# Performance work log

Measured on AMD Instinct MI355X. Metric: run time of the kernel, lower is better.

Reference implementation:

```python
import jax, jax.numpy as jnp
import numpy as np

E = 64            # embedding_size
N = 131072        # total nodes (64 states x 2048 objects)
B = 64            # number of states (for readout)
NUM_LAYERS = 2
SMOOTH = 12.0     # MAXIMUM_SMOOTHNESS
RELS = (("r1", 1, 400_000), ("r2", 2, 400_000), ("r3", 3, 150_000))  # (name, arity, n_atoms)


def mish(x):
    return x * jnp.tanh(jax.nn.softplus(x))


def mlp(x, Wi, bi, Wo, bo):
    # MLP: outer(mish(inner(x)))
    return mish(x @ Wi + bi) @ Wo + bo


def setup_inputs() -> dict:
    key = jax.random.key(0)
    ks = iter(jax.random.split(key, 64))

    def lin(i, o):
        s = 1.0 / np.sqrt(i)
        return jax.random.uniform(next(ks), (i, o), jnp.float32, -s, s)

    d = {"node_embeddings": jax.random.normal(next(ks), (N, E), jnp.float32)}
    for r, a, m in RELS:
        d[f"atoms_{r}"] = jax.random.randint(next(ks), (m * a,), 0, N, jnp.int32)
    d["token_sizes"] = jnp.full((B,), N // B, jnp.int32)
    for r, a, _ in RELS:
        sz = a * E
        d[f"Wi_{r}"] = lin(sz, sz); d[f"bi_{r}"] = jnp.zeros((sz,), jnp.float32)
        d[f"Wo_{r}"] = lin(sz, sz); d[f"bo_{r}"] = jnp.zeros((sz,), jnp.float32)
    d["uWi"] = lin(2 * E, 2 * E); d["ubi"] = jnp.zeros((2 * E,), jnp.float32)
    d["uWo"] = lin(2 * E, E);     d["ubo"] = jnp.zeros((E,), jnp.float32)
    for p in ("v", "d"):
        d[f"{p}Wi"] = lin(E, E); d[f"{p}bi"] = jnp.zeros((E,), jnp.float32)
        d[f"{p}Wo"] = lin(E, 1); d[f"{p}bo"] = jnp.zeros((1,), jnp.float32)
    return d


def _layer(h, atoms, rp, uWi, ubi, uWo, ubo):
    # per-relation gather -> residual MLP -> flatten back to per-term messages
    msg_list, idx_list = [], []
    for (r, a, _) in RELS:
        idx = atoms[r]                                  # [m*a] int node ids
        Wi, bi, Wo, bo = rp[r]
        x = h[idx].reshape(-1, a * E)                   # [m, a*E]
        y = x + mlp(x, Wi, bi, Wo, bo)                  # residual relation MLP
        msg_list.append(y.reshape(-1, E))               # [m*a, E]
        idx_list.append(idx)
    msgs = jnp.concatenate(msg_list, 0)                 # [T, E]
    idxs = jnp.concatenate(idx_list, 0)                 # [T]

    # smooth-max aggregation (torch: index_reduce amax under no_grad + stabilized exp-sum-log)
    cnt = jax.ops.segment_sum(jnp.ones((idxs.shape[0], 1), msgs.dtype), idxs, num_segments=N)
    seg_max = jax.ops.segment_max(msgs, idxs, num_segments=N)     # -inf for empty segments
    exps_max = jax.lax.stop_gradient(jnp.where(cnt > 0, seg_max, 0.0))  # include_self=False; empty nodes stay 0
    exps = jnp.exp(SMOOTH * (msgs - exps_max[idxs]))
    exps_sum = 1e-16 + jax.ops.segment_sum(exps, idxs, num_segments=N)
    max_msg = jnp.log(exps_sum) / SMOOTH + exps_max     # [N, E]

    return h + mlp(jnp.concatenate([max_msg, h], 1), uWi, ubi, uWo, ubo)


def _readout(h, token_sizes, Wi, bi, Wo, bo):
    # SumReadout: cumsum-diff segment sums over states, then MLP -> scalar per state
    ci = jnp.cumsum(token_sizes) - 1
    cs = jnp.cumsum(h, axis=0)[ci]                      # [B, E] cumulative sums at segment ends
    agg = jnp.concatenate([cs[:1], cs[1:] - cs[:-1]], 0)
    return mlp(agg, Wi, bi, Wo, bo).reshape(-1)


def _forward(node_embeddings, atoms, token_sizes, params):
    (rp, uWi, ubi, uWo, ubo, vWi, vbi, vWo, vbo, dWi, dbi, dWo, dbo) = params
    h = node_embeddings
    for _ in range(NUM_LAYERS):
        h = _layer(h, atoms, rp, uWi, ubi, uWo, ubo)
    values = _readout(h, token_sizes, vWi, vbi, vWo, vbo)
    deadends = _readout(h, token_sizes, dWi, dbi, dWo, dbo)
    return values, deadends


def reference(node_embeddings, atoms_r1, atoms_r2, atoms_r3, token_sizes,
              Wi_r1, bi_r1, Wo_r1, bo_r1,
              Wi_r2, bi_r2, Wo_r2, bo_r2,
              Wi_r3, bi_r3, Wo_r3, bo_r3,
              uWi, ubi, uWo, ubo,
              vWi, vbi, vWo, vbo,
              dWi, dbi, dWo, dbo):
    atoms = {"r1": atoms_r1, "r2": atoms_r2, "r3": atoms_r3}
    rp = {"r1": (Wi_r1, bi_r1, Wo_r1, bo_r1),
          "r2": (Wi_r2, bi_r2, Wo_r2, bo_r2),
          "r3": (Wi_r3, bi_r3, Wo_r3, bo_r3)}
    params = (rp, uWi, ubi, uWo, ubo, vWi, vbi, vWo, vbo, dWi, dbi, dWo, dbo)
    return _forward(node_embeddings, atoms, token_sizes, params)
```

## Files before the change

### kernel.cpp

```cpp
#include <hip/hip_runtime.h>
#include <math.h>

#define N_NODES 131072
#define NSTATES 64
#define NH ((size_t)N_NODES * 64)

typedef short bf16x8 __attribute__((ext_vector_type(8)));
typedef float f32x4 __attribute__((ext_vector_type(4)));

__device__ __forceinline__ ushort f2bf(float f) {
    unsigned u = __float_as_uint(f);
    return (ushort)((u + 0x7fffu + ((u >> 16) & 1u)) >> 16);
}
__device__ __forceinline__ float bf2f(ushort h) {
    return __uint_as_float(((unsigned)h) << 16);
}
__device__ __forceinline__ float mishf(float x) {
    if (x > 30.f) return x;
    float t = __builtin_amdgcn_exp2f(1.4426950408889634f * x);
    float r = t * t + 2.f * t;
    return x * r * __builtin_amdgcn_rcpf(r + 2.f);
}
__device__ __forceinline__ unsigned enc_f(float f) {
    unsigned u = __float_as_uint(f);
    return (u & 0x80000000u) ? ~u : (u | 0x80000000u);
}
__device__ __forceinline__ float dec_f(unsigned k) {
    unsigned u = (k & 0x80000000u) ? (k & 0x7fffffffu) : ~k;
    return __uint_as_float(u);
}

__device__ __forceinline__ bf16x8 load8f(const float* p) {
    const float4* q = (const float4*)p;
    float4 v0 = q[0], v1 = q[1];
    bf16x8 u;
    u[0] = (short)f2bf(v0.x); u[1] = (short)f2bf(v0.y);
    u[2] = (short)f2bf(v0.z); u[3] = (short)f2bf(v0.w);
    u[4] = (short)f2bf(v1.x); u[5] = (short)f2bf(v1.y);
    u[6] = (short)f2bf(v1.z); u[7] = (short)f2bf(v1.w);
    return u;
}

__global__ __launch_bounds__(256) void h2bf_kernel(
    const float* __restrict__ h, ushort* __restrict__ hb)
{
    size_t i = ((size_t)blockIdx.x * 256 + threadIdx.x) * 8;
    if (i >= NH) return;
    *(bf16x8*)(hb + i) = load8f(h + i);
}

struct WtJob  { const float* src; ushort* dst; int K; int Nc; int start; };
struct WtJobs { WtJob j[8]; int total; };

__global__ __launch_bounds__(256) void wt_conv_all_kernel(WtJobs jobs)
{
    int i = blockIdx.x * 256 + threadIdx.x;
    if (i >= jobs.total) return;
    int jj = 0;
    #pragma unroll
    for (int k = 1; k < 8; k++) if (i >= jobs.j[k].start) jj = k;
    WtJob jb = jobs.j[jj];
    int local = i - jb.start;
    int o = local / jb.K, k = local % jb.K;
    jb.dst[(size_t)o * jb.K + k] = f2bf(jb.src[(size_t)k * jb.Nc + o]);
}

__global__ __launch_bounds__(256) void count_kernel(
    const int* __restrict__ atoms, int T, unsigned* __restrict__ cnt)
{
    int i = blockIdx.x * 256 + threadIdx.x;
    if (i < T) atomicAdd(&cnt[atoms[i]], 1u);
}

__global__ __launch_bounds__(256) void scan1_kernel(
    const unsigned* __restrict__ cnt, unsigned* __restrict__ base,
    unsigned* __restrict__ totals)
{
    __shared__ unsigned sm[256];
    int t = threadIdx.x, blk = blockIdx.x;
    int i0 = blk * 512;
    unsigned a = cnt[i0 + 2 * t], bb = cnt[i0 + 2 * t + 1];
    unsigned p = a + bb;
    sm[t] = p;
    __syncthreads();
    for (int off = 1; off < 256; off <<= 1) {
        unsigned v = (t >= off) ? sm[t - off] : 0u;
        __syncthreads();
        sm[t] += v;
        __syncthreads();
    }
    unsigned incl = sm[t];
    base[i0 + 2 * t]     = incl - p;
    base[i0 + 2 * t + 1] = incl - p + a;
    if (t == 255) totals[blk] = sm[255];
}

__global__ __launch_bounds__(256) void scan2_kernel(
    unsigned* __restrict__ base, unsigned* __restrict__ pos,
    const unsigned* __restrict__ totals)
{
    __shared__ unsigned ps[4];
    int t = threadIdx.x, blk = blockIdx.x;
    int lane = t & 63, wv = t >> 6;
    unsigned v = (t < blk) ? totals[t] : 0u;
    #pragma unroll
    for (int o = 32; o >= 1; o >>= 1) v += (unsigned)__shfl_xor((int)v, o);
    if (lane == 0) ps[wv] = v;
    __syncthreads();
    unsigned off = ps[0] + ps[1] + ps[2] + ps[3];
    int i0 = blk * 512;
    unsigned b0 = base[i0 + 2 * t] + off;
    unsigned b1 = base[i0 + 2 * t + 1] + off;
    base[i0 + 2 * t]     = b0;  pos[i0 + 2 * t]     = b0;
    base[i0 + 2 * t + 1] = b1;  pos[i0 + 2 * t + 1] = b1;
}

template<int ARITY, int MODE>
__global__ __launch_bounds__(256, (ARITY == 3) ? 3 : 4)
void rel_kernel(const ushort* __restrict__ h, const int* __restrict__ atoms,
                const ushort* __restrict__ WiT, const float* __restrict__ bi,
                const ushort* __restrict__ WoT, const float* __restrict__ bo,
                unsigned* __restrict__ pos, ushort* __restrict__ y_sorted,
                unsigned* __restrict__ enc, float* __restrict__ exps, int m)
{
    constexpr int AE  = ARITY * 64;
    constexpr int BM  = 64;
    constexpr int NTW = AE / 64;
    constexpr int KS  = AE / 32;
    constexpr int S   = AE * 2;
    __shared__ __align__(16) ushort xs[BM * AE];
    __shared__ __align__(16) ushort ts[BM * AE];
    __shared__ unsigned slot_sm[BM * ARITY];
    const int tid = threadIdx.x, lane = tid & 63, wv = tid >> 6;
    const int a0 = blockIdx.x * BM;

    for (int task = tid; task < BM * (AE / 8); task += 256) {
        int r  = task / (AE / 8);
        int c8 = task % (AE / 8);
        int atom = a0 + r;
        bf16x8 u = {0, 0, 0, 0, 0, 0, 0, 0};
        if (atom < m) {
            int node = atoms[atom * ARITY + (c8 >> 3)];
            u = *(const bf16x8*)(h + (size_t)node * 64 + (size_t)(c8 & 7) * 8);
        }
        *(bf16x8*)((char*)xs + r * S + ((c8 * 16) ^ ((r & 7) << 4))) = u;
    }
    __syncthreads();

    const int cw0 = wv * NTW * 16;
    const int kg  = (lane >> 4) * 8;
    const int cl  = lane & 15;

    f32x4 acc[4][NTW];
    #pragma unroll
    for (int n = 0; n < NTW; n++) {
        float b = bi[cw0 + n * 16 + cl];
        #pragma unroll
        for (int a = 0; a < 4; a++) acc[a][n] = (f32x4){b, b, b, b};
    }
    #pragma unroll
    for (int ks = 0; ks < KS; ks++) {
        bf16x8 bf[NTW];
        #pragma unroll
        for (int n = 0; n < NTW; n++)
            bf[n] = *(const bf16x8*)(WiT + (size_t)(cw0 + n * 16 + cl) * AE + ks * 32 + kg);
        #pragma unroll
        for (int a = 0; a < 4; a++) {
            int row = a * 16 + cl;
            bf16x8 af = *(const bf16x8*)((char*)xs + row * S + (((ks * 32 + kg) * 2) ^ ((row & 7) << 4)));
            #pragma unroll
            for (int n = 0; n < NTW; n++)
                acc[a][n] = __builtin_amdgcn_mfma_f32_16x16x32_bf16(af, bf[n], acc[a][n], 0, 0, 0);
        }
    }
    #pragma unroll
    for (int a = 0; a < 4; a++)
        #pragma unroll
        for (int n = 0; n < NTW; n++)
            #pragma unroll
            for (int j = 0; j < 4; j++) {
                int row = a * 16 + (lane >> 4) * 4 + j;
                int col = cw0 + n * 16 + cl;
                *(ushort*)((char*)ts + row * S + ((col * 2) ^ ((row & 7) << 4))) = f2bf(mishf(acc[a][n][j]));
            }
    __syncthreads();

    #pragma unroll
    for (int n = 0; n < NTW; n++) {
        float b = bo[cw0 + n * 16 + cl];
        #pragma unroll
        for (int a = 0; a < 4; a++) acc[a][n] = (f32x4){b, b, b, b};
    }
    #pragma unroll
    for (int ks = 0; ks < KS; ks++) {
        bf16x8 bf[NTW];
        #pragma unroll
        for (int n = 0; n < NTW; n++)
            bf[n] = *(const bf16x8*)(WoT + (size_t)(cw0 + n * 16 + cl) * AE + ks * 32 + kg);
        #pragma unroll
        for (int a = 0; a < 4; a++) {
            int row = a * 16 + cl;
            bf16x8 af = *(const bf16x8*)((char*)ts + row * S + (((ks * 32 + kg) * 2) ^ ((row & 7) << 4)));
            #pragma unroll
            for (int n = 0; n < NTW; n++)
                acc[a][n] = __builtin_amdgcn_mfma_f32_16x16x32_bf16(af, bf[n], acc[a][n], 0, 0, 0);
        }
    }
    #pragma unroll
    for (int a = 0; a < 4; a++)
        #pragma unroll
        for (int n = 0; n < NTW; n++)
            #pragma unroll
            for (int j = 0; j < 4; j++) {
                int row = a * 16 + (lane >> 4) * 4 + j;
                int col = cw0 + n * 16 + cl;
                ushort* xp = (ushort*)((char*)xs + row * S + ((col * 2) ^ ((row & 7) << 4)));
                *xp = f2bf(bf2f(*xp) + acc[a][n][j]);
            }
    __syncthreads();

    const int nrows = BM * ARITY;
    if (MODE == 0) {
        if (tid < nrows) {
            int grow = a0 * ARITY + tid;
            unsigned s = 0u;
            if (grow < m * ARITY) s = atomicAdd(&pos[atoms[grow]], 1u);
            slot_sm[tid] = s;
        }
        __syncthreads();
        for (int rr = wv; rr < nrows; rr += 4) {
            int grow = a0 * ARITY + rr;
            if (grow >= m * ARITY) break;
            int r = rr / ARITY, c = (rr % ARITY) * 64 + lane;
            ushort yu = *(ushort*)((char*)xs + r * S + ((c * 2) ^ ((r & 7) << 4)));
            y_sorted[(size_t)slot_sm[rr] * 64 + lane] = yu;
        }
    } else {
        for (int rr = wv; rr < nrows; rr += 4) {
            int grow = a0 * ARITY + rr;
            if (grow >= m * ARITY) break;
            int node = atoms[grow];
            int r = rr / ARITY, c = (rr % ARITY) * 64 + lane;
            ushort yu = *(ushort*)((char*)xs + r * S + ((c * 2) ^ ((r & 7) << 4)));
            if (MODE == 1) {
                atomicMax(&enc[(size_t)node * 64 + lane], enc_f(bf2f(yu)));
            } else {
                size_t cell = (size_t)node * 64 + lane;
                float mx = dec_f(enc[cell]);
                atomicAdd(&exps[cell], __builtin_amdgcn_exp2f(17.312340490667562f * (bf2f(yu) - mx)));
            }
        }
    }
}

__global__ __launch_bounds__(256) void aggregate_kernel(
    const ushort* __restrict__ y_sorted, const unsigned* __restrict__ base,
    const unsigned* __restrict__ cnt, unsigned* __restrict__ pos,
    ushort* __restrict__ mm)
{
    int node = blockIdx.x * 4 + (threadIdx.x >> 6);
    int lane = threadIdx.x & 63;
    unsigned b = base[node], c = cnt[node];
    if (lane == 0) pos[node] = b;
    const ushort* p = y_sorted + (size_t)b * 64 + lane;
    float mx = -3.402823466e38f;
    for (unsigned j = 0; j < c; j++)
        mx = fmaxf(mx, bf2f(p[(size_t)j * 64]));
    float me = c ? mx : 0.f;
    float s = 0.f;
    for (unsigned j = 0; j < c; j++)
        s += __builtin_amdgcn_exp2f(17.312340490667562f * (bf2f(p[(size_t)j * 64]) - me));
    float r = __builtin_amdgcn_logf(1e-16f + s) * 0.05776226504666211f + me;
    mm[(size_t)node * 64 + lane] = f2bf(r);
}

__global__ __launch_bounds__(256) void finalize_mm_kernel(
    const unsigned* __restrict__ enc, const float* __restrict__ exps,
    ushort* __restrict__ mm)
{
    size_t i = (size_t)blockIdx.x * 256 + threadIdx.x;
    if (i >= NH) return;
    unsigned key = enc[i];
    float mx = key ? dec_f(key) : 0.f;
    float r = __builtin_amdgcn_logf(1e-16f + exps[i]) * 0.05776226504666211f + mx;
    mm[i] = f2bf(r);
}

__global__ __launch_bounds__(256, 4)
void update_kernel(ushort* __restrict__ hio, const ushort* __restrict__ mm,
                   const ushort* __restrict__ uWiT, const float* __restrict__ ubi,
                   const ushort* __restrict__ uWoT, const float* __restrict__ ubo)
{
    constexpr int AE = 128, BM = 64, S = 256, NTW = 2, KS = 4;
    __shared__ __align__(16) ushort xs[BM * AE];
    __shared__ __align__(16) ushort ts[BM * AE];
    const int tid = threadIdx.x, lane = tid & 63, wv = tid >> 6;
    const int n0 = blockIdx.x * BM;

    for (int task = tid; task < BM * 16; task += 256) {
        int r = task >> 4, c8 = task & 15;
        int node = n0 + r;
        bf16x8 u;
        if (c8 < 8) u = *(const bf16x8*)(mm  + (size_t)node * 64 + c8 * 8);
        else        u = *(const bf16x8*)(hio + (size_t)node * 64 + (size_t)(c8 - 8) * 8);
        *(bf16x8*)((char*)xs + r * S + ((c8 * 16) ^ ((r & 7) << 4))) = u;
    }
    __syncthreads();

    const int cw0 = wv * NTW * 16;
    const int kg  = (lane >> 4) * 8;
    const int cl  = lane & 15;

    f32x4 acc[4][NTW];
    #pragma unroll
    for (int n = 0; n < NTW; n++) {
        float b = ubi[cw0 + n * 16 + cl];
        #pragma unroll
        for (int a = 0; a < 4; a++) acc[a][n] = (f32x4){b, b, b, b};
    }
    #pragma unroll
    for (int ks = 0; ks < KS; ks++) {
        bf16x8 bf[NTW];
        #pragma unroll
        for (int n = 0; n < NTW; n++)
            bf[n] = *(const bf16x8*)(uWiT + (size_t)(cw0 + n * 16 + cl) * AE + ks * 32 + kg);
        #pragma unroll
        for (int a = 0; a < 4; a++) {
            int row = a * 16 + cl;
            bf16x8 af = *(const bf16x8*)((char*)xs + row * S + (((ks * 32 + kg) * 2) ^ ((row & 7) << 4)));
            #pragma unroll
            for (int n = 0; n < NTW; n++)
                acc[a][n] = __builtin_amdgcn_mfma_f32_16x16x32_bf16(af, bf[n], acc[a][n], 0, 0, 0);
        }
    }
    #pragma unroll
    for (int a = 0; a < 4; a++)
        #pragma unroll
        for (int n = 0; n < NTW; n++)
            #pragma unroll
            for (int j = 0; j < 4; j++) {
                int row = a * 16 + (lane >> 4) * 4 + j;
                int col = cw0 + n * 16 + cl;
                *(ushort*)((char*)ts + row * S + ((col * 2) ^ ((row & 7) << 4))) = f2bf(mishf(acc[a][n][j]));
            }
    __syncthreads();

    f32x4 acc2[4];
    {
        float b = ubo[wv * 16 + cl];
        #pragma unroll
        for (int a = 0; a < 4; a++) acc2[a] = (f32x4){b, b, b, b};
    }
    #pragma unroll
    for (int ks = 0; ks < KS; ks++) {
        bf16x8 bf = *(const bf16x8*)(uWoT + (size_t)(wv * 16 + cl) * AE + ks * 32 + kg);
        #pragma unroll
        for (int a = 0; a < 4; a++) {
            int row = a * 16 + cl;
            bf16x8 af = *(const bf16x8*)((char*)ts + row * S + (((ks * 32 + kg) * 2) ^ ((row & 7) << 4)));
            acc2[a] = __builtin_amdgcn_mfma_f32_16x16x32_bf16(af, bf, acc2[a], 0, 0, 0);
        }
    }
    #pragma unroll
    for (int a = 0; a < 4; a++)
        #pragma unroll
        for (int j = 0; j < 4; j++) {
            int row = a * 16 + (lane >> 4) * 4 + j;
            int col = wv * 16 + cl;
            int hc = 64 + col;
            float hold = bf2f(*(ushort*)((char*)xs + row * S + ((hc * 2) ^ ((row & 7) << 4))));
            hio[(size_t)(n0 + row) * 64 + col] = f2bf(hold + acc2[a][j]);
        }
}

__global__ __launch_bounds__(64) void offsets_kernel(
    const int* __restrict__ toksz, int* __restrict__ off)
{
    int lane = threadIdx.x;
    int v = toksz[lane];
    int inc = v;
    #pragma unroll
    for (int o = 1; o < 64; o <<= 1) {
        int t = __shfl_up(inc, o);
        if (lane >= o) inc += t;
    }
    off[lane] = inc - v;
}

#define RCHUNK 32
__global__ __launch_bounds__(256) void readout_partial_kernel(
    const ushort* __restrict__ h, const int* __restrict__ toksz,
    const int* __restrict__ off, float* __restrict__ part)
{
    int s = blockIdx.x >> 5, c = blockIdx.x & (RCHUNK - 1);
    int cntr = toksz[s];
    int rpc = (cntr + RCHUNK - 1) / RCHUNK;
    int r0 = c * rpc;
    int r1 = min(r0 + rpc, cntr);
    int col = threadIdx.x & 63, rg = threadIdx.x >> 6;
    int base = off[s];
    float acc = 0.f;
    for (int r = r0 + rg; r < r1; r += 4)
        acc += bf2f(h[(size_t)(base + r) * 64 + col]);
    __shared__ float red[4][64];
    red[rg][col] = acc;
    __syncthreads();
    if (rg == 0)
        part[(size_t)blockIdx.x * 64 + col] = red[0][col] + red[1][col] + red[2][col] + red[3][col];
}

__global__ __launch_bounds__(256) void readout_reduce_kernel(
    const float* __restrict__ part, float* __restrict__ agg)
{
    int s = blockIdx.x;
    int col = threadIdx.x & 63, rg = threadIdx.x >> 6;
    float acc = 0.f;
    for (int k = rg; k < RCHUNK; k += 4)
        acc += part[(size_t)(s * RCHUNK + k) * 64 + col];
    __shared__ float red[4][64];
    red[rg][col] = acc;
    __syncthreads();
    if (rg == 0)
        agg[s * 64 + col] = red[0][col] + red[1][col] + red[2][col] + red[3][col];
}

__global__ __launch_bounds__(64) void readout_mlp_kernel(
    const float* __restrict__ agg,
    const float* __restrict__ vWi, const float* __restrict__ vbi,
    const float* __restrict__ vWo, const float* __restrict__ vbo,
    const float* __restrict__ dWi, const float* __restrict__ dbi,
    const float* __restrict__ dWo, const float* __restrict__ dbo,
    float* __restrict__ out)
{
    int s = blockIdx.x;
    int lane = threadIdx.x;
    float accv = vbi[lane], accd = dbi[lane];
    for (int k = 0; k < 64; k++) {
        float a = agg[s * 64 + k];
        accv = fmaf(a, vWi[k * 64 + lane], accv);
        accd = fmaf(a, dWi[k * 64 + lane], accd);
    }
    float pv = mishf(accv) * vWo[lane];
    float pd = mishf(accd) * dWo[lane];
    #pragma unroll
    for (int o = 1; o < 64; o <<= 1) {
        pv += __shfl_xor(pv, o);
        pd += __shfl_xor(pd, o);
    }
    if (lane == 0) { out[s] = pv + vbo[0]; out[64 + s] = pd + dbo[0]; }
}

extern "C" void kernel_launch(void* const* d_in, const int* in_sizes, int n_in,
                              void* d_out, int out_size, void* d_ws, size_t ws_size,
                              hipStream_t stream)
{
    const float* h0   = (const float*)d_in[0];
    const int* atoms1 = (const int*)d_in[1];
    const int* atoms2 = (const int*)d_in[2];
    const int* atoms3 = (const int*)d_in[3];
    const int* tsizes = (const int*)d_in[4];
    const float* Wi1 = (const float*)d_in[5],  *bi1 = (const float*)d_in[6];
    const float* Wo1 = (const float*)d_in[7],  *bo1 = (const float*)d_in[8];
    const float* Wi2 = (const float*)d_in[9],  *bi2 = (const float*)d_in[10];
    const float* Wo2 = (const float*)d_in[11], *bo2 = (const float*)d_in[12];
    const float* Wi3 = (const float*)d_in[13], *bi3 = (const float*)d_in[14];
    const float* Wo3 = (const float*)d_in[15], *bo3 = (const float*)d_in[16];
    const float* uWi = (const float*)d_in[17], *ubi = (const float*)d_in[18];
    const float* uWo = (const float*)d_in[19], *ubo = (const float*)d_in[20];
    const float* vWi = (const float*)d_in[21], *vbi = (const float*)d_in[22];
    const float* vWo = (const float*)d_in[23], *vbo = (const float*)d_in[24];
    const float* dWi = (const float*)d_in[25], *dbi = (const float*)d_in[26];
    const float* dWo = (const float*)d_in[27], *dbo = (const float*)d_in[28];
    float* out = (float*)d_out;

    const int rows1 = in_sizes[1];
    const int rows2 = in_sizes[2];
    const int rows3 = in_sizes[3];
    const int m1 = rows1, m2 = rows2 / 2, m3 = rows3 / 3;
    const int T = rows1 + rows2 + rows3;

    char* w = (char*)d_ws;
    auto alloc = [&](size_t bytes) { char* p = w; w += (bytes + 255) & ~(size_t)255; return p; };
    ushort* h1       = (ushort*)alloc(NH * 2);
    ushort* mm       = (ushort*)alloc(NH * 2);
    unsigned* cnt    = (unsigned*)alloc(N_NODES * 4);
    unsigned* base   = (unsigned*)alloc(N_NODES * 4);
    unsigned* pos    = (unsigned*)alloc(N_NODES * 4);
    unsigned* totals = (unsigned*)alloc(256 * 4);
    float* agg       = (float*)alloc(NSTATES * 64 * 4);
    float* part      = (float*)alloc((size_t)NSTATES * RCHUNK * 64 * 4);
    int* roff        = (int*)alloc(NSTATES * 4);
    ushort* WiT1 = (ushort*)alloc(64 * 64 * 2);
    ushort* WoT1 = (ushort*)alloc(64 * 64 * 2);
    ushort* WiT2 = (ushort*)alloc(128 * 128 * 2);
    ushort* WoT2 = (ushort*)alloc(128 * 128 * 2);
    ushort* WiT3 = (ushort*)alloc(192 * 192 * 2);
    ushort* WoT3 = (ushort*)alloc(192 * 192 * 2);
    ushort* uWiT = (ushort*)alloc(128 * 128 * 2);
    ushort* uWoT = (ushort*)alloc(64 * 128 * 2);
    char* tail = w;

    size_t y_bytes  = (size_t)T * 64 * 2;
    const bool csr  = ((size_t)(tail - (char*)d_ws) + ((y_bytes + 255) & ~(size_t)255)) <= ws_size;
    ushort* y_sorted = nullptr;
    unsigned* enc = nullptr;
    float* exps = nullptr;
    if (csr) {
        y_sorted = (ushort*)alloc(y_bytes);
    } else {
        enc  = (unsigned*)alloc(NH * 4);
        exps = (float*)alloc(NH * 4);
    }

    h2bf_kernel<<<(int)(NH / 8 / 256), 256, 0, stream>>>(h0, h1);

    {
        WtJobs jobs;
        int s = 0;
        auto add = [&](int idx, const float* src, ushort* dst, int K, int Nc) {
            jobs.j[idx] = {src, dst, K, Nc, s};
            s += K * Nc;
        };
        add(0, Wi1, WiT1, 64, 64);
        add(1, Wo1, WoT1, 64, 64);
        add(2, Wi2, WiT2, 128, 128);
        add(3, Wo2, WoT2, 128, 128);
        add(4, Wi3, WiT3, 192, 192);
        add(5, Wo3, WoT3, 192, 192);
        add(6, uWi, uWiT, 128, 128);
        add(7, uWo, uWoT, 128, 64);
        jobs.total = s;
        wt_conv_all_kernel<<<(s + 255) / 256, 256, 0, stream>>>(jobs);
    }

    if (csr) {
        hipMemsetAsync(cnt, 0, N_NODES * 4, stream);
        count_kernel<<<(rows1 + 255) / 256, 256, 0, stream>>>(atoms1, rows1, cnt);
        count_kernel<<<(rows2 + 255) / 256, 256, 0, stream>>>(atoms2, rows2, cnt);
        count_kernel<<<(rows3 + 255) / 256, 256, 0, stream>>>(atoms3, rows3, cnt);
        scan1_kernel<<<256, 256, 0, stream>>>(cnt, base, totals);
        scan2_kernel<<<256, 256, 0, stream>>>(base, pos, totals);
    }

    const int g1 = (m1 + 63) / 64, g2 = (m2 + 63) / 64, g3 = (m3 + 63) / 64;

    for (int layer = 0; layer < 2; layer++) {
        if (csr) {
            rel_kernel<1, 0><<<g1, 256, 0, stream>>>(h1, atoms1, WiT1, bi1, WoT1, bo1, pos, y_sorted, nullptr, nullptr, m1);
            rel_kernel<2, 0><<<g2, 256, 0, stream>>>(h1, atoms2, WiT2, bi2, WoT2, bo2, pos, y_sorted, nullptr, nullptr, m2);
            rel_kernel<3, 0><<<g3, 256, 0, stream>>>(h1, atoms3, WiT3, bi3, WoT3, bo3, pos, y_sorted, nullptr, nullptr, m3);
            aggregate_kernel<<<N_NODES / 4, 256, 0, stream>>>(y_sorted, base, cnt, pos, mm);
        } else {
            hipMemsetAsync(enc, 0, NH * 8, stream);
            rel_kernel<1, 1><<<g1, 256, 0, stream>>>(h1, atoms1, WiT1, bi1, WoT1, bo1, nullptr, nullptr, enc, exps, m1);
            rel_kernel<2, 1><<<g2, 256, 0, stream>>>(h1, atoms2, WiT2, bi2, WoT2, bo2, nullptr, nullptr, enc, exps, m2);
            rel_kernel<3, 1><<<g3, 256, 0, stream>>>(h1, atoms3, WiT3, bi3, WoT3, bo3, nullptr, nullptr, enc, exps, m3);
            rel_kernel<1, 2><<<g1, 256, 0, stream>>>(h1, atoms1, WiT1, bi1, WoT1, bo1, nullptr, nullptr, enc, exps, m1);
            rel_kernel<2, 2><<<g2, 256, 0, stream>>>(h1, atoms2, WiT2, bi2, WoT2, bo2, nullptr, nullptr, enc, exps, m2);
            rel_kernel<3, 2><<<g3, 256, 0, stream>>>(h1, atoms3, WiT3, bi3, WoT3, bo3, nullptr, nullptr, enc, exps, m3);
            finalize_mm_kernel<<<(int)((NH + 255) / 256), 256, 0, stream>>>(enc, exps, mm);
        }
        update_kernel<<<N_NODES / 64, 256, 0, stream>>>(h1, mm, uWiT, ubi, uWoT, ubo);
    }

    offsets_kernel<<<1, 64, 0, stream>>>(tsizes, roff);
    readout_partial_kernel<<<NSTATES * RCHUNK, 256, 0, stream>>>(h1, tsizes, roff, part);
    readout_reduce_kernel<<<NSTATES, 256, 0, stream>>>(part, agg);
    readout_mlp_kernel<<<NSTATES, 64, 0, stream>>>(agg, vWi, vbi, vWo, vbo,
                                                   dWi, dbi, dWo, dbo, out);
}
```

Measured before the change: 829.5 us.

## Precompute CSR slots once and use online-softmax vectorized aggregation

Scatter slot assignment moves out of the per-layer relation kernels into a one-time rank pass that stores each term's destination slot, so the atomics are no longer repeated in every layer and no longer need resetting. The aggregate kernel now uses a block of 256 threads per 4 nodes with 16-byte vector loads and a single-pass online max/exp-sum, combined through shuffles and shared memory. This replaces the previous one-wave-per-node two-pass scan. It costs an extra slot array, and the aggregation adds more exp evaluations and block syncs per node.

```diff
diff --git a/kernel.cpp b/kernel.cpp
--- a/kernel.cpp
+++ b/kernel.cpp
@@ -115,12 +115,20 @@
     base[i0 + 2 * t + 1] = b1;  pos[i0 + 2 * t + 1] = b1;
 }
 
+__global__ __launch_bounds__(256) void rank_kernel(
+    const int* __restrict__ atoms, int T, unsigned* __restrict__ pos,
+    unsigned* __restrict__ slot)
+{
+    int i = blockIdx.x * 256 + threadIdx.x;
+    if (i < T) slot[i] = atomicAdd(&pos[atoms[i]], 1u);
+}
+
 template<int ARITY, int MODE>
 __global__ __launch_bounds__(256, (ARITY == 3) ? 3 : 4)
 void rel_kernel(const ushort* __restrict__ h, const int* __restrict__ atoms,
                 const ushort* __restrict__ WiT, const float* __restrict__ bi,
                 const ushort* __restrict__ WoT, const float* __restrict__ bo,
-                unsigned* __restrict__ pos, ushort* __restrict__ y_sorted,
+                const unsigned* __restrict__ slot, ushort* __restrict__ y_sorted,
                 unsigned* __restrict__ enc, float* __restrict__ exps, int m)
 {
     constexpr int AE  = ARITY * 64;
@@ -130,7 +138,6 @@
     constexpr int S   = AE * 2;
     __shared__ __align__(16) ushort xs[BM * AE];
     __shared__ __align__(16) ushort ts[BM * AE];
-    __shared__ unsigned slot_sm[BM * ARITY];
     const int tid = threadIdx.x, lane = tid & 63, wv = tid >> 6;
     const int a0 = blockIdx.x * BM;
 
@@ -220,58 +227,104 @@
     __syncthreads();
 
     const int nrows = BM * ARITY;
-    if (MODE == 0) {
-        if (tid < nrows) {
-            int grow = a0 * ARITY + tid;
-            unsigned s = 0u;
-            if (grow < m * ARITY) s = atomicAdd(&pos[atoms[grow]], 1u);
-            slot_sm[tid] = s;
-        }
-        __syncthreads();
-        for (int rr = wv; rr < nrows; rr += 4) {
-            int grow = a0 * ARITY + rr;
-            if (grow >= m * ARITY) break;
-            int r = rr / ARITY, c = (rr % ARITY) * 64 + lane;
-            ushort yu = *(ushort*)((char*)xs + r * S + ((c * 2) ^ ((r & 7) << 4)));
-            y_sorted[(size_t)slot_sm[rr] * 64 + lane] = yu;
-        }
-    } else {
-        for (int rr = wv; rr < nrows; rr += 4) {
-            int grow = a0 * ARITY + rr;
-            if (grow >= m * ARITY) break;
+    for (int rr = wv; rr < nrows; rr += 4) {
+        int grow = a0 * ARITY + rr;
+        if (grow >= m * ARITY) break;
+        int r = rr / ARITY, c = (rr % ARITY) * 64 + lane;
+        ushort yu = *(ushort*)((char*)xs + r * S + ((c * 2) ^ ((r & 7) << 4)));
+        if (MODE == 0) {
+            unsigned sl = slot[grow];
+            y_sorted[(size_t)sl * 64 + lane] = yu;
+        } else if (MODE == 1) {
             int node = atoms[grow];
-            int r = rr / ARITY, c = (rr % ARITY) * 64 + lane;
-            ushort yu = *(ushort*)((char*)xs + r * S + ((c * 2) ^ ((r & 7) << 4)));
-            if (MODE == 1) {
-                atomicMax(&enc[(size_t)node * 64 + lane], enc_f(bf2f(yu)));
-            } else {
-                size_t cell = (size_t)node * 64 + lane;
-                float mx = dec_f(enc[cell]);
-                atomicAdd(&exps[cell], __builtin_amdgcn_exp2f(17.312340490667562f * (bf2f(yu) - mx)));
-            }
-        }
-    }
-}
-
+            atomicMax(&enc[(size_t)node * 64 + lane], enc_f(bf2f(yu)));
+        } else {
+            int node = atoms[grow];
+            size_t cell = (size_t)node * 64 + lane;
+            float mx = dec_f(enc[cell]);
+            atomicAdd(&exps[cell], __builtin_amdgcn_exp2f(17.312340490667562f * (bf2f(yu) - mx)));
+        }
+    }
+}
+
+#define KSM 17.312340490667562f
+#define NEGBIG -3.402823466e38f
 __global__ __launch_bounds__(256) void aggregate_kernel(
     const ushort* __restrict__ y_sorted, const unsigned* __restrict__ base,
-    const unsigned* __restrict__ cnt, unsigned* __restrict__ pos,
-    ushort* __restrict__ mm)
-{
-    int node = blockIdx.x * 4 + (threadIdx.x >> 6);
-    int lane = threadIdx.x & 63;
-    unsigned b = base[node], c = cnt[node];
-    if (lane == 0) pos[node] = b;
-    const ushort* p = y_sorted + (size_t)b * 64 + lane;
-    float mx = -3.402823466e38f;
-    for (unsigned j = 0; j < c; j++)
-        mx = fmaxf(mx, bf2f(p[(size_t)j * 64]));
-    float me = c ? mx : 0.f;
-    float s = 0.f;
-    for (unsigned j = 0; j < c; j++)
-        s += __builtin_amdgcn_exp2f(17.312340490667562f * (bf2f(p[(size_t)j * 64]) - me));
-    float r = __builtin_amdgcn_logf(1e-16f + s) * 0.05776226504666211f + me;
-    mm[(size_t)node * 64 + lane] = f2bf(r);
+    const unsigned* __restrict__ cnt, ushort* __restrict__ mm)
+{
+    const int n0 = blockIdx.x * 4;
+    const int tid = threadIdx.x;
+    const int colg = tid & 7;
+    const int rowg = tid >> 3;
+    const int lane = tid & 63, wv = tid >> 6;
+
+    __shared__ float red_m[4][8][8];
+    __shared__ float red_s[4][8][8];
+
+    for (int nd = 0; nd < 4; nd++) {
+        const unsigned bs = base[n0 + nd], c = cnt[n0 + nd];
+        float m_[8], s_[8];
+        #pragma unroll
+        for (int k = 0; k < 8; k++) { m_[k] = NEGBIG; s_[k] = 0.f; }
+
+        for (unsigned r = rowg; r < c; r += 32) {
+            bf16x8 v = *(const bf16x8*)(y_sorted + (size_t)(bs + r) * 64 + colg * 8);
+            #pragma unroll
+            for (int k = 0; k < 8; k++) {
+                float a  = bf2f((ushort)v[k]);
+                float mn = fmaxf(m_[k], a);
+                s_[k] = s_[k] * __builtin_amdgcn_exp2f(KSM * (m_[k] - mn))
+                      + __builtin_amdgcn_exp2f(KSM * (a - mn));
+                m_[k] = mn;
+            }
+        }
+        #pragma unroll
+        for (int off = 8; off <= 32; off <<= 1) {
+            #pragma unroll
+            for (int k = 0; k < 8; k++) {
+                float mo = __shfl_xor(m_[k], off);
+                float so = __shfl_xor(s_[k], off);
+                float mn = fmaxf(m_[k], mo);
+                s_[k] = s_[k] * __builtin_amdgcn_exp2f(KSM * (m_[k] - mn))
+                      + so   * __builtin_amdgcn_exp2f(KSM * (mo   - mn));
+                m_[k] = mn;
+            }
+        }
+        if ((lane >> 3) == 0) {
+            #pragma unroll
+            for (int k = 0; k < 8; k++) {
+                red_m[wv][lane][k] = m_[k];
+                red_s[wv][lane][k] = s_[k];
+            }
+        }
+        __syncthreads();
+        if (tid < 8) {
+            float M[8], Sv[8];
+            #pragma unroll
+            for (int k = 0; k < 8; k++) { M[k] = red_m[0][tid][k]; Sv[k] = red_s[0][tid][k]; }
+            #pragma unroll
+            for (int wvi = 1; wvi < 4; wvi++) {
+                #pragma unroll
+                for (int k = 0; k < 8; k++) {
+                    float mo = red_m[wvi][tid][k], so = red_s[wvi][tid][k];
+                    float mn = fmaxf(M[k], mo);
+                    Sv[k] = Sv[k] * __builtin_amdgcn_exp2f(KSM * (M[k] - mn))
+                          + so    * __builtin_amdgcn_exp2f(KSM * (mo   - mn));
+                    M[k] = mn;
+                }
+            }
+            bf16x8 o;
+            #pragma unroll
+            for (int k = 0; k < 8; k++) {
+                float me = c ? M[k] : 0.f;
+                float r = __builtin_amdgcn_logf(1e-16f + Sv[k]) * 0.05776226504666211f + me;
+                o[k] = (short)f2bf(r);
+            }
+            *(bf16x8*)(mm + (size_t)(n0 + nd) * 64 + tid * 8) = o;
+        }
+        __syncthreads();
+    }
 }
 
 __global__ __launch_bounds__(256) void finalize_mm_kernel(
@@ -487,6 +540,7 @@
     unsigned* base   = (unsigned*)alloc(N_NODES * 4);
     unsigned* pos    = (unsigned*)alloc(N_NODES * 4);
     unsigned* totals = (unsigned*)alloc(256 * 4);
+    unsigned* slot   = (unsigned*)alloc((size_t)T * 4);
     float* agg       = (float*)alloc(NSTATES * 64 * 4);
     float* part      = (float*)alloc((size_t)NSTATES * RCHUNK * 64 * 4);
     int* roff        = (int*)alloc(NSTATES * 4);
@@ -511,6 +565,9 @@
         enc  = (unsigned*)alloc(NH * 4);
         exps = (float*)alloc(NH * 4);
     }
+    unsigned* slot1 = slot;
+    unsigned* slot2 = slot + rows1;
+    unsigned* slot3 = slot + rows1 + rows2;
 
     h2bf_kernel<<<(int)(NH / 8 / 256), 256, 0, stream>>>(h0, h1);
 
@@ -540,16 +597,19 @@
         count_kernel<<<(rows3 + 255) / 256, 256, 0, stream>>>(atoms3, rows3, cnt);
         scan1_kernel<<<256, 256, 0, stream>>>(cnt, base, totals);
         scan2_kernel<<<256, 256, 0, stream>>>(base, pos, totals);
+        rank_kernel<<<(rows1 + 255) / 256, 256, 0, stream>>>(atoms1, rows1, pos, slot1);
+        rank_kernel<<<(rows2 + 255) / 256, 256, 0, stream>>>(atoms2, rows2, pos, slot2);
+        rank_kernel<<<(rows3 + 255) / 256, 256, 0, stream>>>(atoms3, rows3, pos, slot3);
     }
 
     const int g1 = (m1 + 63) / 64, g2 = (m2 + 63) / 64, g3 = (m3 + 63) / 64;
 
     for (int layer = 0; layer < 2; layer++) {
         if (csr) {
-            rel_kernel<1, 0><<<g1, 256, 0, stream>>>(h1, atoms1, WiT1, bi1, WoT1, bo1, pos, y_sorted, nullptr, nullptr, m1);
-            rel_kernel<2, 0><<<g2, 256, 0, stream>>>(h1, atoms2, WiT2, bi2, WoT2, bo2, pos, y_sorted, nullptr, nullptr, m2);
-            rel_kernel<3, 0><<<g3, 256, 0, stream>>>(h1, atoms3, WiT3, bi3, WoT3, bo3, pos, y_sorted, nullptr, nullptr, m3);
-            aggregate_kernel<<<N_NODES / 4, 256, 0, stream>>>(y_sorted, base, cnt, pos, mm);
+            rel_kernel<1, 0><<<g1, 256, 0, stream>>>(h1, atoms1, WiT1, bi1, WoT1, bo1, slot1, y_sorted, nullptr, nullptr, m1);
+            rel_kernel<2, 0><<<g2, 256, 0, stream>>>(h1, atoms2, WiT2, bi2, WoT2, bo2, slot2, y_sorted, nullptr, nullptr, m2);
+            rel_kernel<3, 0><<<g3, 256, 0, stream>>>(h1, atoms3, WiT3, bi3, WoT3, bo3, slot3, y_sorted, nullptr, nullptr, m3);
+            aggregate_kernel<<<N_NODES / 4, 256, 0, stream>>>(y_sorted, base, cnt, mm);
         } else {
             hipMemsetAsync(enc, 0, NH * 8, stream);
             rel_kernel<1, 1><<<g1, 256, 0, stream>>>(h1, atoms1, WiT1, bi1, WoT1, bo1, nullptr, nullptr, enc, exps, m1);
```

New measurement: 1.540 ms. 85.7% more time.
